# Performance work log

Measured on AMD Instinct MI355X. Metric: run time of the kernel, lower is better.

Reference implementation:

```python
import jax, jax.numpy as jnp
import numpy as np

D_MODEL = 1024
NUM_HEADS = 16
DEPTH = D_MODEL // NUM_HEADS
BATCH = 2
SEQ = 2048


def setup_inputs() -> dict:
    key = jax.random.key(0)
    ks = jax.random.split(key, 12)
    s = 1.0 / np.sqrt(D_MODEL)
    inp = {
        'v': jax.random.normal(ks[0], (BATCH, SEQ, D_MODEL), jnp.float32),
        'k': jax.random.normal(ks[1], (BATCH, SEQ, D_MODEL), jnp.float32),
        'q': jax.random.normal(ks[2], (BATCH, SEQ, D_MODEL), jnp.float32),
        # causal mask: 1.0 where attention is disallowed (strict upper triangle)
        'mask': jnp.triu(jnp.ones((1, 1, SEQ, SEQ), jnp.float32), k=1),
        'Wq': jax.random.normal(ks[3], (D_MODEL, D_MODEL), jnp.float32) * s,
        'bq': jnp.zeros((D_MODEL,), jnp.float32),
        'Wk': jax.random.normal(ks[4], (D_MODEL, D_MODEL), jnp.float32) * s,
        'bk': jnp.zeros((D_MODEL,), jnp.float32),
        'Wv': jax.random.normal(ks[5], (D_MODEL, D_MODEL), jnp.float32) * s,
        'bv': jnp.zeros((D_MODEL,), jnp.float32),
        'Wo': jax.random.normal(ks[6], (D_MODEL, D_MODEL), jnp.float32) * s,
        'bo': jnp.zeros((D_MODEL,), jnp.float32),
    }
    return inp


def _split_heads(x):
    b, s, _ = x.shape
    return x.reshape(b, s, NUM_HEADS, DEPTH).transpose(0, 2, 1, 3)  # [B,H,S,Dh]


def reference(v, k, q, mask, Wq, bq, Wk, bk, Wv, bv, Wo, bo):
    b = q.shape[0]
    qh = _split_heads(q @ Wq.T + bq)
    kh = _split_heads(k @ Wk.T + bk)
    vh = _split_heads(v @ Wv.T + bv)
    scores = jnp.einsum('bhsd,bhtd->bhst', qh, kh) / jnp.sqrt(
        jnp.asarray(DEPTH, jnp.float32))
    scores = scores + mask * (-1e9)
    attn = jax.nn.softmax(scores, axis=-1)
    out = jnp.einsum('bhst,bhtd->bhsd', attn, vh)
    out = out.transpose(0, 2, 1, 3).reshape(b, -1, D_MODEL)
    return out @ Wo.T + bo
```

## Files before the change

### kernel.cpp

```cpp
#include <hip/hip_runtime.h>
#include <hip/hip_bf16.h>

#define D_MODEL 1024
#define NHEADS 16
#define DEPTH 64
#define BATCH 2
#define SEQ 2048
#define NTOK (BATCH * SEQ)

#define QSCALE 0.180336884f
#define DEFER_THR 11.5415603f

typedef short bf16x8 __attribute__((ext_vector_type(8)));
typedef float f32x4 __attribute__((ext_vector_type(4)));
typedef float f32x16 __attribute__((ext_vector_type(16)));
typedef unsigned short ushortx8 __attribute__((ext_vector_type(8)));
typedef unsigned uint2v __attribute__((ext_vector_type(2)));

using gas_ptr = const __attribute__((address_space(1))) unsigned int*;
using las_ptr = __attribute__((address_space(3))) unsigned int*;

__device__ __forceinline__ unsigned short f2bf(float f) {
    union { float f; unsigned u; } v; v.f = f;
    unsigned r = v.u + 0x7fffu + ((v.u >> 16) & 1u);
    return (unsigned short)(r >> 16);
}

__device__ __forceinline__ unsigned cvtpk(float lo, float hi) {
    unsigned r;
    asm("v_cvt_pk_bf16_f32 %0, %1, %2" : "=v"(r) : "v"(lo), "v"(hi));
    return r;
}

__device__ __forceinline__ uint2v pls(unsigned a, unsigned b) {
    return __builtin_amdgcn_permlane32_swap(a, b, false, false);
}

__device__ __forceinline__ void gload16(const void* g, void* l) {
    __builtin_amdgcn_global_load_lds((gas_ptr)g, (las_ptr)l, 16, 0, 0);
}

__global__ __launch_bounds__(256) void convert_w(
    const float* __restrict__ wq, const float* __restrict__ wk,
    const float* __restrict__ wv, const float* __restrict__ wo,
    unsigned short* __restrict__ wqb, unsigned short* __restrict__ wkb,
    unsigned short* __restrict__ wvb, unsigned short* __restrict__ wob)
{
    const int WT = (D_MODEL * D_MODEL) / 8;
    const int total = 4 * WT;
    for (int i = blockIdx.x * 256 + threadIdx.x; i < total; i += gridDim.x * 256) {
        int wsel = i >> 17, off = i & (WT - 1);
        const float* s = (wsel == 0) ? wq : (wsel == 1) ? wk : (wsel == 2) ? wv : wo;
        unsigned short* d = (wsel == 0) ? wqb : (wsel == 1) ? wkb : (wsel == 2) ? wvb : wob;
        float sc = (wsel == 0) ? QSCALE : 1.f;
        float4 a = ((const float4*)s)[off * 2];
        float4 b = ((const float4*)s)[off * 2 + 1];
        ushortx8 r;
        r[0] = f2bf(a.x * sc); r[1] = f2bf(a.y * sc);
        r[2] = f2bf(a.z * sc); r[3] = f2bf(a.w * sc);
        r[4] = f2bf(b.x * sc); r[5] = f2bf(b.y * sc);
        r[6] = f2bf(b.z * sc); r[7] = f2bf(b.w * sc);
        ((ushortx8*)d)[off] = r;
    }
}

template<int IT, int DEST, bool QKV, bool AF32>
__global__ __launch_bounds__(256) void gemm_bf16(
    const void* __restrict__ A0v, const void* __restrict__ A1v,
    const void* __restrict__ A2v,
    const unsigned short* __restrict__ B0, const unsigned short* __restrict__ B1,
    const unsigned short* __restrict__ B2,
    const float* __restrict__ bias0, const float* __restrict__ bias1,
    const float* __restrict__ bias2,
    void* __restrict__ C0, void* __restrict__ C1, void* __restrict__ C2,
    int M, int N, int K)
{
    constexpr int BM = IT * 32;
    constexpr int WROWS = IT * 16;
    __shared__ float          Asf[AF32 ? 2 * BM * 32 : 4];
    __shared__ unsigned short As16[AF32 ? 4 : 2 * BM * 32];
    __shared__ unsigned short Bs[2 * 128 * 32];

    const void* Av = A0v; const unsigned short* Bw = B0;
    const float* bias = bias0;    void* Cp = C0;
    float bsc = 1.f;
    int zz = 0;
    if (QKV) {
        zz = blockIdx.z;
        if (zz == 0) bsc = QSCALE;
        if (zz == 1) { Av = A1v; Bw = B1; bias = bias1; Cp = C1; }
        else if (zz == 2) { Av = A2v; Bw = B2; bias = bias2; Cp = C2; }
    }

    const int tid  = threadIdx.x;
    const int lane = tid & 63;
    const int w    = tid >> 6;
    const int wu   = __builtin_amdgcn_readfirstlane(w);
    const int wr   = w >> 1, wc = w & 1;
    const int lr   = lane & 15, lg = lane >> 4;

    const int row0 = blockIdx.x * BM;
    const int n0   = blockIdx.y * 128;

    const int cB0 = wu * 64 + lane;
    const unsigned short* gB0 = Bw + (size_t)(n0 + (cB0 >> 2)) * K + (cB0 & 3) * 8;
    const unsigned short* gB1 = Bw + (size_t)(n0 + 64 + (cB0 >> 2)) * K + (cB0 & 3) * 8;

    const float* Af = (const float*)Av;
    const unsigned short* Ab = (const unsigned short*)Av;

    const float* gAf[4];
    if (AF32) {
#pragma unroll
        for (int cc = 0; cc < 4; ++cc) {
            int p = (cc * 4 + wu) * 64 + lane;
            int r_ = p >> 3, s_ = p & 7;
            gAf[cc] = Af + (size_t)(row0 + r_) * K + (size_t)((s_ ^ (r_ & 7)) * 4);
        }
    }
    const unsigned short* gA0 = nullptr;
    const unsigned short* gA1 = nullptr;
    if (!AF32) {
        gA0 = Ab + (size_t)(row0 + (cB0 >> 2)) * K + (cB0 & 3) * 8;
        if (IT == 4)
            gA1 = Ab + (size_t)(row0 + 64 + (cB0 >> 2)) * K + (cB0 & 3) * 8;
    }

    auto STAGE = [&](int kt, int buf) {
        if constexpr (AF32) {
#pragma unroll
            for (int cc = 0; cc < 4; ++cc)
                gload16(gAf[cc] + kt, &Asf[buf * (BM * 32) + (cc * 4 + wu) * 256]);
        } else {
            gload16(gA0 + kt, &As16[buf * (BM * 32) + wu * 512]);
            if (IT == 4) gload16(gA1 + kt, &As16[buf * (BM * 32) + 2048 + wu * 512]);
        }
        gload16(gB0 + kt, &Bs[buf * 4096 + wu * 512]);
        gload16(gB1 + kt, &Bs[buf * 4096 + 2048 + wu * 512]);
    };

    f32x4 acc[IT][4];
    for (int i = 0; i < IT; ++i)
        for (int j = 0; j < 4; ++j)
            for (int r = 0; r < 4; ++r) acc[i][j][r] = 0.f;

    STAGE(0, 0);
    __syncthreads();

    const int NT = K / 32;
    int cur = 0;
    for (int t = 0; t < NT; ++t) {
        if (t + 1 < NT) STAGE((t + 1) * 32, cur ^ 1);

        bf16x8 af[IT], bfr[4];
#pragma unroll
        for (int i = 0; i < IT; ++i) {
            const int arow = wr * WROWS + i * 16 + lr;
            if constexpr (AF32) {
                const int x_ = arow & 7;
                const int s0_ = (lg * 2) ^ x_;
                const int s1_ = (lg * 2 + 1) ^ x_;
                f32x4 lo4 = *(const f32x4*)&Asf[cur * (BM * 32) + arow * 32 + s0_ * 4];
                f32x4 hi4 = *(const f32x4*)&Asf[cur * (BM * 32) + arow * 32 + s1_ * 4];
                union { unsigned u[4]; bf16x8 v; } uu;
                uu.u[0] = cvtpk(lo4[0], lo4[1]);
                uu.u[1] = cvtpk(lo4[2], lo4[3]);
                uu.u[2] = cvtpk(hi4[0], hi4[1]);
                uu.u[3] = cvtpk(hi4[2], hi4[3]);
                af[i] = uu.v;
            } else {
                af[i] = *(const bf16x8*)&As16[cur * (BM * 32) + arow * 32 + lg * 8];
            }
        }
#pragma unroll
        for (int j = 0; j < 4; ++j)
            bfr[j] = *(const bf16x8*)&Bs[cur * 4096 + (wc * 64 + j * 16 + lr) * 32 + lg * 8];
#pragma unroll
        for (int i = 0; i < IT; ++i)
#pragma unroll
            for (int j = 0; j < 4; ++j)
                acc[i][j] = __builtin_amdgcn_mfma_f32_16x16x32_bf16(
                    af[i], bfr[j], acc[i][j], 0, 0, 0);

        __syncthreads();
        cur ^= 1;
    }

    for (int i = 0; i < IT; ++i) {
        for (int j = 0; j < 4; ++j) {
            int gcol = n0 + wc * 64 + j * 16 + lr;
            float bv = bias[gcol] * bsc;
            int s0full = row0 + wr * WROWS + i * 16 + lg * 4;
            if (QKV && zz == 1) {
                int b_ = s0full >> 11, sr = s0full & (SEQ - 1);
                int h_ = gcol >> 6, dh = gcol & 63;
                int jt_ = sr >> 6, t0 = sr & 63;
                int tb_ = t0 >> 5, m0 = t0 & 31;
                int dk_ = dh >> 4, hi_ = (dh >> 3) & 1, e_ = dh & 7;
                unsigned short* Kf = (unsigned short*)Cp;
                size_t base = ((size_t)(b_ * NHEADS + h_) * (SEQ >> 6) + jt_) * 4096
                            + (size_t)((tb_ * 4 + dk_) * 64 + hi_ * 32) * 8 + e_;
#pragma unroll
                for (int r = 0; r < 4; ++r)
                    Kf[base + (size_t)(m0 + r) * 8] = f2bf(acc[i][j][r] + bv);
            } else if (QKV && zz == 2) {
                int b_ = s0full >> 11, sr = s0full & (SEQ - 1);
                int h_ = gcol >> 6, dh = gcol & 63;
                int jt_ = sr >> 6, t0 = sr & 63;
                int ts_ = t0 >> 4, hi_ = (t0 >> 3) & 1, e0 = t0 & 7;
                int dblk = dh >> 5, m_ = dh & 31;
                unsigned w0 = (unsigned)f2bf(acc[i][j][0] + bv)
                            | ((unsigned)f2bf(acc[i][j][1] + bv) << 16);
                unsigned w1 = (unsigned)f2bf(acc[i][j][2] + bv)
                            | ((unsigned)f2bf(acc[i][j][3] + bv) << 16);
                unsigned long long pk = (unsigned long long)w0
                                      | ((unsigned long long)w1 << 32);
                unsigned short* Vf = (unsigned short*)Cp;
                size_t idx = ((size_t)(b_ * NHEADS + h_) * (SEQ >> 6) + jt_) * 4096
                           + (size_t)((dblk * 4 + ts_) * 64 + hi_ * 32 + m_) * 8 + e0;
                *(unsigned long long*)&Vf[idx] = pk;
            } else if (DEST == 0) {
#pragma unroll
                for (int r = 0; r < 4; ++r) {
                    int grow = s0full + r;
                    float val = acc[i][j][r] + bv;
                    int b_ = grow >> 11, s = grow & (SEQ - 1);
                    int h_ = gcol >> 6, dh = gcol & 63;
                    ((unsigned short*)Cp)[(((size_t)b_ * NHEADS + h_) * SEQ + s) * DEPTH + dh]
                        = f2bf(val);
                }
            } else {
#pragma unroll
                for (int r = 0; r < 4; ++r) {
                    int grow = s0full + r;
                    ((float*)Cp)[(size_t)grow * N + gcol] = acc[i][j][r] + bv;
                }
            }
        }
    }
}

#define KLOAD(JT, KF)                                                          \
{                                                                              \
    const unsigned short* Kt_ = Kb + (size_t)(JT) * 4096;                      \
    _Pragma("unroll")                                                          \
    for (int f_ = 0; f_ < 8; ++f_)                                             \
        KF[f_] = *(const bf16x8*)&Kt_[(size_t)f_ * 512 + lane * 8];            \
}

#define TILE_BODY(KC, KN)                                                      \
{                                                                              \
    const unsigned short* Vg = Vb + (size_t)jt * 4096;                         \
    bf16x8 vf0[4], vf1[4];                                                     \
    _Pragma("unroll")                                                          \
    for (int ts = 0; ts < 4; ++ts) {                                           \
        vf0[ts] = *(const bf16x8*)&Vg[(size_t)ts * 512 + lane * 8];            \
        vf1[ts] = *(const bf16x8*)&Vg[(size_t)(4 + ts) * 512 + lane * 8];      \
    }                                                                          \
    if (jt + 2 < ntiles) { KLOAD(jt + 2, KN) }                                 \
    f32x16 st[2];                                                              \
    __builtin_amdgcn_s_setprio(1);                                             \
    _Pragma("unroll")                                                          \
    for (int tb = 0; tb < 2; ++tb) {                                           \
        f32x16 a;                                                              \
        _Pragma("unroll") for (int r = 0; r < 16; ++r) a[r] = 0.f;             \
        _Pragma("unroll")                                                      \
        for (int dk = 0; dk < 4; ++dk)                                         \
            a = __builtin_amdgcn_mfma_f32_32x32x16_bf16(KC[tb * 4 + dk], qf[dk], a, 0, 0, 0); \
        st[tb] = a;                                                            \
    }                                                                          \
    __builtin_amdgcn_s_setprio(0);                                             \
    if (jt == ntiles - 1) {                                                    \
        _Pragma("unroll")                                                      \
        for (int tb = 0; tb < 2; ++tb)                                         \
            _Pragma("unroll")                                                  \
            for (int r = 0; r < 16; ++r) {                                     \
                int t = jt * 64 + tb * 32 + (r & 3) + 8 * (r >> 2) + 4 * hi;   \
                if (t > qr0 + m) st[tb][r] = -1e9f;                            \
            }                                                                  \
    }                                                                          \
    float tmx[16];                                                             \
    _Pragma("unroll")                                                          \
    for (int r = 0; r < 16; ++r) tmx[r] = fmaxf(st[0][r], st[1][r]);           \
    _Pragma("unroll")                                                          \
    for (int sft = 8; sft; sft >>= 1)                                          \
        _Pragma("unroll")                                                      \
        for (int r = 0; r < 8; ++r)                                            \
            if (r < sft) tmx[r] = fmaxf(tmx[r], tmx[r + sft]);                 \
    float tmax;                                                                \
    {                                                                          \
        union { float f; unsigned u; } cu_; cu_.f = tmx[0];                    \
        uint2v rr_ = pls(cu_.u, cu_.u);                                        \
        union { unsigned u; float f; } a_, b_; a_.u = rr_[0]; b_.u = rr_[1];   \
        tmax = fmaxf(a_.f, b_.f);                                              \
    }                                                                          \
    if (!__all(tmax <= mrun + DEFER_THR)) {                                    \
        float mnew = fmaxf(mrun, tmax);                                        \
        float sc = exp2f(mrun - mnew);                                         \
        mrun = mnew; lrun *= sc;                                               \
        if (hi == 0) scbw[m] = sc;                                             \
        f32x4 s4[4];                                                           \
        _Pragma("unroll")                                                      \
        for (int g = 0; g < 4; ++g) s4[g] = *(f32x4*)&scbw[g * 8 + hi * 4];    \
        _Pragma("unroll")                                                      \
        for (int r = 0; r < 16; ++r) {                                         \
            float f = s4[r >> 2][r & 3];                                       \
            o0[r] *= f; o1[r] *= f;                                            \
        }                                                                      \
    }                                                                          \
    _Pragma("unroll")                                                          \
    for (int tb = 0; tb < 2; ++tb)                                             \
        _Pragma("unroll")                                                      \
        for (int r = 0; r < 16; ++r)                                           \
            st[tb][r] = exp2f(st[tb][r] - mrun);                               \
    float s16[16];                                                             \
    _Pragma("unroll")                                                          \
    for (int r = 0; r < 16; ++r) s16[r] = st[0][r] + st[1][r];                 \
    _Pragma("unroll")                                                          \
    for (int sft = 8; sft; sft >>= 1)                                          \
        _Pragma("unroll")                                                      \
        for (int r = 0; r < 8; ++r)                                            \
            if (r < sft) s16[r] += s16[r + sft];                               \
    {                                                                          \
        union { float f; unsigned u; } cu_; cu_.f = s16[0];                    \
        uint2v rr_ = pls(cu_.u, cu_.u);                                        \
        union { unsigned u; float f; } a_, b_; a_.u = rr_[0]; b_.u = rr_[1];   \
        lrun += a_.f + b_.f;                                                   \
    }                                                                          \
    unsigned pkw[8][2];                                                        \
    _Pragma("unroll")                                                          \
    for (int G = 0; G < 8; ++G) {                                              \
        const int tb = G >> 2, g = G & 3;                                      \
        pkw[G][0] = cvtpk(st[tb][4 * g + 0], st[tb][4 * g + 1]);               \
        pkw[G][1] = cvtpk(st[tb][4 * g + 2], st[tb][4 * g + 3]);               \
    }                                                                          \
    __builtin_amdgcn_s_setprio(1);                                             \
    _Pragma("unroll")                                                          \
    for (int ts = 0; ts < 4; ++ts) {                                           \
        uint2v s0_ = pls(pkw[2 * ts][0], pkw[2 * ts + 1][0]);                  \
        uint2v s1_ = pls(pkw[2 * ts][1], pkw[2 * ts + 1][1]);                  \
        union { unsigned u[4]; bf16x8 v; } uu;                                 \
        uu.u[0] = s0_[0]; uu.u[1] = s1_[0]; uu.u[2] = s0_[1]; uu.u[3] = s1_[1]; \
        o0 = __builtin_amdgcn_mfma_f32_32x32x16_bf16(uu.v, vf0[ts], o0, 0, 0, 0); \
        o1 = __builtin_amdgcn_mfma_f32_32x32x16_bf16(uu.v, vf1[ts], o1, 0, 0, 0); \
    }                                                                          \
    __builtin_amdgcn_s_setprio(0);                                             \
}

__global__ __launch_bounds__(128, 2) void attn_wave(
    const unsigned short* __restrict__ Qh, const unsigned short* __restrict__ Kh,
    const unsigned short* __restrict__ Vt, unsigned short* __restrict__ ctx)
{
    __shared__ __align__(16) float scb[2][32];
    __shared__ __align__(16) float mlbuf[2][2][32];
    __shared__ __align__(16) float c0b[32], c1b[32], invb[32];
    __shared__ __align__(16) float osh0[16][64], osh1[16][64];

    const int tid  = threadIdx.x;
    const int ww   = tid >> 6;
    const int lane = tid & 63;
    const int m    = lane & 31;
    const int hi   = lane >> 5;
    float* scbw = scb[ww];

    const int bid  = blockIdx.x;
    const int bh   = bid & 31;
    const int qb   = 63 - (bid >> 5);
    const int qr0  = qb * 32;

    const int b = bh >> 4, h = bh & 15;
    const unsigned short* Qb = Qh + ((size_t)bh * SEQ + qr0) * DEPTH;
    const unsigned short* Kb = Kh + (size_t)bh * SEQ * DEPTH;
    const unsigned short* Vb = Vt + (size_t)bh * SEQ * DEPTH;

    bf16x8 qf[4];
#pragma unroll
    for (int dk = 0; dk < 4; ++dk)
        qf[dk] = *(const bf16x8*)&Qb[(size_t)m * DEPTH + dk * 16 + hi * 8];

    f32x16 o0, o1;
#pragma unroll
    for (int r = 0; r < 16; ++r) { o0[r] = 0.f; o1[r] = 0.f; }
    float mrun = -1e30f, lrun = 0.f;

    const int ntiles = (qb >> 1) + 1;
    bf16x8 kfA[8], kfB[8];

    int jt = ww;
    if (jt < ntiles) {
        KLOAD(jt, kfA)
        while (true) {
            TILE_BODY(kfA, kfB)
            jt += 2; if (jt >= ntiles) break;
            TILE_BODY(kfB, kfA)
            jt += 2; if (jt >= ntiles) break;
        }
    }

    if (hi == 0) { mlbuf[ww][0][m] = mrun; mlbuf[ww][1][m] = lrun; }
    __syncthreads();
    if (ww == 0 && hi == 0) {
        float m0 = mlbuf[0][0][m], l0 = mlbuf[0][1][m];
        float m1 = mlbuf[1][0][m], l1 = mlbuf[1][1][m];
        float M  = fmaxf(m0, m1);
        float c0 = exp2f(m0 - M), c1 = exp2f(m1 - M);
        c0b[m] = c0; c1b[m] = c1;
        invb[m] = 1.0f / (l0 * c0 + l1 * c1);
    }
    __syncthreads();

    const float* cb = (ww == 0) ? c0b : c1b;
    f32x4 fc[4];
#pragma unroll
    for (int g = 0; g < 4; ++g)
        fc[g] = *(const f32x4*)&cb[g * 8 + hi * 4];
#pragma unroll
    for (int r = 0; r < 16; ++r) {
        float f = fc[r >> 2][r & 3];
        o0[r] *= f; o1[r] *= f;
    }
    if (ww == 0) {
#pragma unroll
        for (int r = 0; r < 16; ++r) { osh0[r][lane] = o0[r]; osh1[r][lane] = o1[r]; }
    }
    __syncthreads();
    if (ww == 1) {
        f32x4 fi[4];
#pragma unroll
        for (int g = 0; g < 4; ++g)
            fi[g] = *(const f32x4*)&invb[g * 8 + hi * 4];
#pragma unroll
        for (int r = 0; r < 16; ++r) {
            float inv = fi[r >> 2][r & 3];
            int ml = (r & 3) + 8 * (r >> 2) + 4 * hi;
            size_t rowbase = ((size_t)b * SEQ + qr0 + ml) * D_MODEL + h * DEPTH;
            ctx[rowbase + m]      = f2bf((o0[r] + osh0[r][lane]) * inv);
            ctx[rowbase + 32 + m] = f2bf((o1[r] + osh1[r][lane]) * inv);
        }
    }
}

extern "C" void kernel_launch(void* const* d_in, const int* in_sizes, int n_in,
                              void* d_out, int out_size, void* d_ws, size_t ws_size,
                              hipStream_t stream) {
    const float* v  = (const float*)d_in[0];
    const float* k  = (const float*)d_in[1];
    const float* q  = (const float*)d_in[2];
    const float* Wq = (const float*)d_in[4];
    const float* bq = (const float*)d_in[5];
    const float* Wk = (const float*)d_in[6];
    const float* bk = (const float*)d_in[7];
    const float* Wv = (const float*)d_in[8];
    const float* bv = (const float*)d_in[9];
    const float* Wo = (const float*)d_in[10];
    const float* bo = (const float*)d_in[11];

    char* ws = (char*)d_ws;
    const size_t MB = 1024 * 1024;
    unsigned short* ctx = (unsigned short*)(ws + 0);
    unsigned short* Wqb = (unsigned short*)(ws + 8  * MB);
    unsigned short* Wkb = (unsigned short*)(ws + 10 * MB);
    unsigned short* Wvb = (unsigned short*)(ws + 12 * MB);
    unsigned short* Wob = (unsigned short*)(ws + 14 * MB);
    unsigned short* Qh  = (unsigned short*)(ws + 16 * MB);
    unsigned short* Kh  = (unsigned short*)(ws + 24 * MB);
    unsigned short* Vtt = (unsigned short*)(ws + 32 * MB);

    convert_w<<<1024, 256, 0, stream>>>(Wq, Wk, Wv, Wo, Wqb, Wkb, Wvb, Wob);

    gemm_bf16<4, 0, true, true><<<dim3(32, 8, 3), 256, 0, stream>>>(
        q, k, v, Wqb, Wkb, Wvb, bq, bk, bv,
        (void*)Qh, (void*)Kh, (void*)Vtt, NTOK, D_MODEL, D_MODEL);

    attn_wave<<<dim3(2048), 128, 0, stream>>>(Qh, Kh, Vtt, ctx);

    gemm_bf16<2, 1, false, false><<<dim3(64, 8), 256, 0, stream>>>(
        ctx, nullptr, nullptr, Wob, nullptr, nullptr, bo, nullptr, nullptr,
        d_out, nullptr, nullptr, NTOK, D_MODEL, D_MODEL);
}
```

Baseline: 113.6 us.

## Use single-buffered 64-wide K tiles instead of double-buffered 32-wide tiles in GEMM

```diff
diff --git a/kernel.cpp b/kernel.cpp
--- a/kernel.cpp
+++ b/kernel.cpp
@@ -77,9 +77,9 @@
 {
     constexpr int BM = IT * 32;
     constexpr int WROWS = IT * 16;
-    __shared__ float          Asf[AF32 ? 2 * BM * 32 : 4];
-    __shared__ unsigned short As16[AF32 ? 4 : 2 * BM * 32];
-    __shared__ unsigned short Bs[2 * 128 * 32];
+    __shared__ float          Asf[AF32 ? BM * 64 : 4];
+    __shared__ unsigned short As16[AF32 ? 4 : BM * 64];
+    __shared__ unsigned short Bs[128 * 64];
 
     const void* Av = A0v; const unsigned short* Bw = B0;
     const float* bias = bias0;    void* Cp = C0;
@@ -102,41 +102,44 @@
     const int row0 = blockIdx.x * BM;
     const int n0   = blockIdx.y * 128;
 
-    const int cB0 = wu * 64 + lane;
-    const unsigned short* gB0 = Bw + (size_t)(n0 + (cB0 >> 2)) * K + (cB0 & 3) * 8;
-    const unsigned short* gB1 = Bw + (size_t)(n0 + 64 + (cB0 >> 2)) * K + (cB0 & 3) * 8;
-
     const float* Af = (const float*)Av;
     const unsigned short* Ab = (const unsigned short*)Av;
-
-    const float* gAf[4];
+    const unsigned short* gBp[4];
+#pragma unroll
+    for (int cc = 0; cc < 4; ++cc) {
+        int p = (cc * 4 + wu) * 64 + lane;
+        gBp[cc] = Bw + (size_t)(n0 + (p >> 3)) * K + (p & 7) * 8;
+    }
+    const float* gAf[IT * 2];
+    const unsigned short* gAb[IT];
     if (AF32) {
 #pragma unroll
-        for (int cc = 0; cc < 4; ++cc) {
+        for (int cc = 0; cc < IT * 2; ++cc) {
             int p = (cc * 4 + wu) * 64 + lane;
-            int r_ = p >> 3, s_ = p & 7;
-            gAf[cc] = Af + (size_t)(row0 + r_) * K + (size_t)((s_ ^ (r_ & 7)) * 4);
-        }
-    }
-    const unsigned short* gA0 = nullptr;
-    const unsigned short* gA1 = nullptr;
-    if (!AF32) {
-        gA0 = Ab + (size_t)(row0 + (cB0 >> 2)) * K + (cB0 & 3) * 8;
-        if (IT == 4)
-            gA1 = Ab + (size_t)(row0 + 64 + (cB0 >> 2)) * K + (cB0 & 3) * 8;
-    }
-
-    auto STAGE = [&](int kt, int buf) {
+            int r_ = p >> 4, s_ = p & 15;
+            gAf[cc] = Af + (size_t)(row0 + r_) * K + (size_t)((s_ ^ (r_ & 15)) * 4);
+        }
+    } else {
+#pragma unroll
+        for (int cc = 0; cc < IT; ++cc) {
+            int p = (cc * 4 + wu) * 64 + lane;
+            gAb[cc] = Ab + (size_t)(row0 + (p >> 3)) * K + (p & 7) * 8;
+        }
+    }
+
+    auto STAGE = [&](int kt) {
         if constexpr (AF32) {
 #pragma unroll
-            for (int cc = 0; cc < 4; ++cc)
-                gload16(gAf[cc] + kt, &Asf[buf * (BM * 32) + (cc * 4 + wu) * 256]);
+            for (int cc = 0; cc < IT * 2; ++cc)
+                gload16(gAf[cc] + kt, &Asf[(cc * 4 + wu) * 256]);
         } else {
-            gload16(gA0 + kt, &As16[buf * (BM * 32) + wu * 512]);
-            if (IT == 4) gload16(gA1 + kt, &As16[buf * (BM * 32) + 2048 + wu * 512]);
-        }
-        gload16(gB0 + kt, &Bs[buf * 4096 + wu * 512]);
-        gload16(gB1 + kt, &Bs[buf * 4096 + 2048 + wu * 512]);
+#pragma unroll
+            for (int cc = 0; cc < IT; ++cc)
+                gload16(gAb[cc] + kt, &As16[(cc * 4 + wu) * 512]);
+        }
+#pragma unroll
+        for (int cc = 0; cc < 4; ++cc)
+            gload16(gBp[cc] + kt, &Bs[(cc * 4 + wu) * 512]);
     };
 
     f32x4 acc[IT][4];
@@ -144,46 +147,49 @@
         for (int j = 0; j < 4; ++j)
             for (int r = 0; r < 4; ++r) acc[i][j][r] = 0.f;
 
-    STAGE(0, 0);
-    __syncthreads();
-
-    const int NT = K / 32;
-    int cur = 0;
+    const int NT = K / 64;
     for (int t = 0; t < NT; ++t) {
-        if (t + 1 < NT) STAGE((t + 1) * 32, cur ^ 1);
-
-        bf16x8 af[IT], bfr[4];
+        STAGE(t * 64);
+        __syncthreads();
+
+        bf16x8 af[IT][2], bfr[4][2];
 #pragma unroll
         for (int i = 0; i < IT; ++i) {
             const int arow = wr * WROWS + i * 16 + lr;
-            if constexpr (AF32) {
-                const int x_ = arow & 7;
-                const int s0_ = (lg * 2) ^ x_;
-                const int s1_ = (lg * 2 + 1) ^ x_;
-                f32x4 lo4 = *(const f32x4*)&Asf[cur * (BM * 32) + arow * 32 + s0_ * 4];
-                f32x4 hi4 = *(const f32x4*)&Asf[cur * (BM * 32) + arow * 32 + s1_ * 4];
-                union { unsigned u[4]; bf16x8 v; } uu;
-                uu.u[0] = cvtpk(lo4[0], lo4[1]);
-                uu.u[1] = cvtpk(lo4[2], lo4[3]);
-                uu.u[2] = cvtpk(hi4[0], hi4[1]);
-                uu.u[3] = cvtpk(hi4[2], hi4[3]);
-                af[i] = uu.v;
-            } else {
-                af[i] = *(const bf16x8*)&As16[cur * (BM * 32) + arow * 32 + lg * 8];
+#pragma unroll
+            for (int kk = 0; kk < 2; ++kk) {
+                if constexpr (AF32) {
+                    const int x_ = arow & 15;
+                    const int s0_ = (kk * 8 + lg * 2) ^ x_;
+                    const int s1_ = (kk * 8 + lg * 2 + 1) ^ x_;
+                    f32x4 lo4 = *(const f32x4*)&Asf[arow * 64 + s0_ * 4];
+                    f32x4 hi4 = *(const f32x4*)&Asf[arow * 64 + s1_ * 4];
+                    union { unsigned u[4]; bf16x8 v; } uu;
+                    uu.u[0] = cvtpk(lo4[0], lo4[1]);
+                    uu.u[1] = cvtpk(lo4[2], lo4[3]);
+                    uu.u[2] = cvtpk(hi4[0], hi4[1]);
+                    uu.u[3] = cvtpk(hi4[2], hi4[3]);
+                    af[i][kk] = uu.v;
+                } else {
+                    af[i][kk] = *(const bf16x8*)&As16[arow * 64 + kk * 32 + lg * 8];
+                }
             }
         }
 #pragma unroll
         for (int j = 0; j < 4; ++j)
-            bfr[j] = *(const bf16x8*)&Bs[cur * 4096 + (wc * 64 + j * 16 + lr) * 32 + lg * 8];
-#pragma unroll
-        for (int i = 0; i < IT; ++i)
-#pragma unroll
-            for (int j = 0; j < 4; ++j)
-                acc[i][j] = __builtin_amdgcn_mfma_f32_16x16x32_bf16(
-                    af[i], bfr[j], acc[i][j], 0, 0, 0);
+#pragma unroll
+            for (int kk = 0; kk < 2; ++kk)
+                bfr[j][kk] = *(const bf16x8*)&Bs[(wc * 64 + j * 16 + lr) * 64 + kk * 32 + lg * 8];
+#pragma unroll
+        for (int kk = 0; kk < 2; ++kk)
+#pragma unroll
+            for (int i = 0; i < IT; ++i)
+#pragma unroll
+                for (int j = 0; j < 4; ++j)
+                    acc[i][j] = __builtin_amdgcn_mfma_f32_16x16x32_bf16(
+                        af[i][kk], bfr[j][kk], acc[i][j], 0, 0, 0);
 
         __syncthreads();
-        cur ^= 1;
     }
 
     for (int i = 0; i < IT; ++i) {
```

Result: slower. 125.2 us (+10.2%).
